# Optimization experiments

Hardware: AMD Instinct MI355X
Metric: run time of the kernel (lower is better)

## Reference

```python
import jax, jax.numpy as jnp
import numpy as np

N_NODES = 50000
N_EDGES = 800000
C_FEAT = 96
HID = 96
C_CONST = 0.005


def _psi(v):
    return jnp.sign(v) * jnp.log(jnp.abs(v) + 1.0)


def setup_inputs() -> dict:
    key = jax.random.key(0)
    ks = jax.random.split(key, 16)
    d_e_in = 2 * C_FEAT + 2
    d_h_in = 2 * C_FEAT
    def w(k, fan_in, fan_out):
        return jax.random.normal(k, (fan_in, fan_out), jnp.float32) * (1.0 / np.sqrt(fan_in))
    return {
        "x": jax.random.normal(ks[0], (N_NODES, 4), jnp.float32),
        "h": jax.random.normal(ks[1], (N_NODES, C_FEAT), jnp.float32),
        "edge_i": jax.random.randint(ks[2], (N_EDGES,), 0, N_NODES, jnp.int32),
        "edge_j": jax.random.randint(ks[3], (N_EDGES,), 0, N_NODES, jnp.int32),
        "We1": w(ks[4], d_e_in, HID), "be1": jnp.zeros((HID,), jnp.float32),
        "We2": w(ks[5], HID, HID), "be2": jnp.zeros((HID,), jnp.float32),
        "Wm": w(ks[6], HID, 1), "bm": jnp.zeros((1,), jnp.float32),
        "Wh1": w(ks[7], d_h_in, HID), "bh1": jnp.zeros((HID,), jnp.float32),
        "Wh2": w(ks[8], HID, C_FEAT), "bh2": jnp.zeros((C_FEAT,), jnp.float32),
        "Wx1": w(ks[9], HID, HID), "bx1": jnp.zeros((HID,), jnp.float32),
        "Wx2": w(ks[10], HID, 1),  # bias-free last phi_x layer
    }


def reference(x, h, edge_i, edge_j, We1, be1, We2, be2, Wm, bm,
              Wh1, bh1, Wh2, bh2, Wx1, bx1, Wx2):
    n = x.shape[0]
    x_i = x[edge_i]            # (K,4)
    x_j = x[edge_j]            # (K,4)
    # Minkowski invariants: 2*t-component - full Euclidean sum == (+,-,-,-)
    d2 = jnp.square(x_i - x_j)
    norms = 2.0 * d2[..., 0] - jnp.sum(d2, axis=-1)
    z = x_i * x_j
    prods = 2.0 * z[..., 0] - jnp.sum(z, axis=-1)
    norms = _psi(norms)[:, None]   # (K,1)
    prods = _psi(prods)[:, None]   # (K,1)

    e_in = jnp.concatenate([h[edge_i], h[edge_j], norms, prods], axis=-1)  # (K,2C+2)
    m = jax.nn.relu(jax.nn.relu(e_in @ We1 + be1) @ We2 + be2)             # (K,HID)
    w_gate = jax.nn.sigmoid(m @ Wm + bm)                                   # (K,1)

    wm = jax.ops.segment_sum(w_gate * m, edge_i, num_segments=n)          # (N,HID)
    dh = jax.nn.relu(jnp.concatenate([h, wm], axis=-1) @ Wh1 + bh1) @ Wh2 + bh2
    h_out = h + dh

    phi_x = jax.nn.relu(m @ Wx1 + bx1) @ Wx2                              # (K,1)
    vals = phi_x * x_j                                                     # (K,4)
    s = jax.ops.segment_sum(vals, edge_i, num_segments=n)                 # (N,4)
    cnt = jax.ops.segment_sum(jnp.ones((vals.shape[0],), vals.dtype), edge_i, num_segments=n)
    mean = jnp.where(cnt[:, None] > 0, s / jnp.maximum(cnt[:, None], 1.0), 0.0)
    x_out = x + C_CONST * mean
    return (h_out, x_out)
```

## Files before the change

kernel.cpp:

```cpp
#include <hip/hip_runtime.h>
#include <math.h>

#define NN 50000
#define NE 800000
#define NB 196
#define TE 128
#define AST 100

typedef __attribute__((ext_vector_type(8))) short short8v;
typedef __attribute__((ext_vector_type(4))) float f32x4;

__device__ __forceinline__ unsigned short f2bf(float f) {
  unsigned u = __float_as_uint(f);
  u += 0x7FFFu + ((u >> 16) & 1u);
  return (unsigned short)(u >> 16);
}
__device__ __forceinline__ unsigned pk2(float a, float b) {
  return (unsigned)f2bf(a) | ((unsigned)f2bf(b) << 16);
}
__device__ __forceinline__ float bflo(unsigned u) { return __uint_as_float(u << 16); }
__device__ __forceinline__ float bfhi(unsigned u) { return __uint_as_float(u & 0xFFFF0000u); }
__device__ __forceinline__ short8v pack8(float4 a, float4 b) {
  short8v r;
  r[0] = (short)f2bf(a.x); r[1] = (short)f2bf(a.y);
  r[2] = (short)f2bf(a.z); r[3] = (short)f2bf(a.w);
  r[4] = (short)f2bf(b.x); r[5] = (short)f2bf(b.y);
  r[6] = (short)f2bf(b.z); r[7] = (short)f2bf(b.w);
  return r;
}

__global__ void kprep(const int* __restrict__ ei, int* __restrict__ cnt,
                      const float* __restrict__ We1, const float* __restrict__ We2,
                      const float* __restrict__ Wx1, const float* __restrict__ Wh1,
                      const float* __restrict__ Wh2,
                      unsigned short* __restrict__ We1p, unsigned short* __restrict__ We2p,
                      unsigned short* __restrict__ Wx1p, unsigned short* __restrict__ Wh1p,
                      unsigned short* __restrict__ Wh2p) {
  const int b = blockIdx.x;
  if (b < NE / 256) {
    const int i = b * 256 + threadIdx.x;
    atomicAdd(&cnt[ei[i]], 1);
    return;
  }
  const int t = (b - NE / 256) * 256 + threadIdx.x;
  const int j = t & 7, lane = (t >> 3) & 63;
  const int kk = (lane >> 4) * 8 + j;
  const int nn = lane & 15;
  {
    const int tile = t >> 9, tk = tile / 12, tn = tile % 12;
    const int k = tk * 32 + kk, n2 = tn * 16 + nn;
    const float v = (n2 < 96) ? We1[k * 96 + n2] : We1[(96 + k) * 96 + (n2 - 96)];
    We1p[t] = f2bf(v);
  }
  {
    const int tile = t >> 9, tk = tile / 6, tn = tile % 6;
    const int k = tk * 32 + kk, n = tn * 16 + nn;
    Wh1p[t] = f2bf(Wh1[k * 96 + n]);
  }
  if (t < 9216) {
    const int tile = t >> 9, tk = tile / 6, tn = tile % 6;
    const int k = tk * 32 + kk, n = tn * 16 + nn;
    We2p[t] = f2bf(We2[k * 96 + n]);
    Wx1p[t] = f2bf(Wx1[k * 96 + n]);
    Wh2p[t] = f2bf(Wh2[k * 96 + n]);
  }
}

__global__ void kscanA(const int* __restrict__ cnt, int* __restrict__ pre,
                       int* __restrict__ bsum) {
  __shared__ int ps[256];
  const int b = blockIdx.x, t = threadIdx.x, idx = b * 256 + t;
  const int v = (idx < NN) ? cnt[idx] : 0;
  ps[t] = v;
  __syncthreads();
  for (int off = 1; off < 256; off <<= 1) {
    const int u = (t >= off) ? ps[t - off] : 0;
    __syncthreads();
    ps[t] += u;
    __syncthreads();
  }
  if (idx < NN) pre[idx] = ps[t] - v;
  if (t == 255) bsum[b] = ps[255];
}

__global__ void kscanB(const int* __restrict__ bsum, int* __restrict__ boff) {
  __shared__ int ps[256];
  const int t = threadIdx.x;
  const int v = (t < NB) ? bsum[t] : 0;
  ps[t] = v;
  __syncthreads();
  for (int off = 1; off < 256; off <<= 1) {
    const int u = (t >= off) ? ps[t - off] : 0;
    __syncthreads();
    ps[t] += u;
    __syncthreads();
  }
  if (t < NB) boff[t] = ps[t] - v;
}

__global__ void kscanC(const int* __restrict__ pre, const int* __restrict__ boff,
                       int* __restrict__ base, int* __restrict__ cursor) {
  const int b = blockIdx.x, t = threadIdx.x, idx = b * 256 + t;
  if (idx < NN) {
    const int v = pre[idx] + boff[b];
    base[idx] = v;
    cursor[idx] = v;
  }
  if (idx == 0) base[NN] = NE;
}

__global__ void kperm(const int* __restrict__ ei, const int* __restrict__ ej,
                      int* __restrict__ cursor,
                      int* __restrict__ eis, int* __restrict__ ejs) {
  const int i = blockIdx.x * 256 + threadIdx.x;
  const int vi = ei[i];
  const int pos = atomicAdd(&cursor[vi], 1);
  eis[pos] = vi;
  ejs[pos] = ej[i];
}

__global__ __launch_bounds__(256, 6) void k0_AB(const float* __restrict__ h,
                                                const unsigned short* __restrict__ We1p,
                                                unsigned short* __restrict__ Abf,
                                                unsigned short* __restrict__ Bbf) {
  __shared__ __align__(16) unsigned short outT[64 * 200];
  const int tid = threadIdx.x;
  const int nb = blockIdx.x * 64;
  const int l = tid & 63, w = tid >> 6, cg = l & 15, rg = l >> 4;
  {
    const int node = nb + w * 16 + cg;
    const int nc = node < NN ? node : NN - 1;
    short8v af[3];
    #pragma unroll
    for (int tk = 0; tk < 3; ++tk) {
      const float* p = h + (size_t)nc * 96 + tk * 32 + rg * 8;
      af[tk] = pack8(*(const float4*)p, *(const float4*)(p + 4));
    }
    const short8v* Wp = (const short8v*)We1p;
    __builtin_amdgcn_s_setprio(1);
    #pragma unroll
    for (int tn = 0; tn < 12; ++tn) {
      f32x4 acc = (f32x4){0.f, 0.f, 0.f, 0.f};
      acc = __builtin_amdgcn_mfma_f32_16x16x32_bf16(af[0], Wp[(0 * 12 + tn) * 64 + l], acc, 0, 0, 0);
      acc = __builtin_amdgcn_mfma_f32_16x16x32_bf16(af[1], Wp[(1 * 12 + tn) * 64 + l], acc, 0, 0, 0);
      acc = __builtin_amdgcn_mfma_f32_16x16x32_bf16(af[2], Wp[(2 * 12 + tn) * 64 + l], acc, 0, 0, 0);
      #pragma unroll
      for (int r = 0; r < 4; ++r)
        outT[(w * 16 + rg * 4 + r) * 200 + tn * 16 + cg] = f2bf(acc[r]);
    }
    __builtin_amdgcn_s_setprio(0);
  }
  __syncthreads();
  {
    const int e = tid & 63, q = tid >> 6;
    const int node = nb + e;
    if (node < NN) {
      const unsigned* src = (const unsigned*)outT + e * 100;
      if (q < 2) {
        uint4* dA = (uint4*)(Abf + (size_t)node * 96);
        #pragma unroll
        for (int i = 0; i < 6; ++i) dA[q * 6 + i] = *(const uint4*)(src + (q * 6 + i) * 4);
      } else {
        uint4* dB = (uint4*)(Bbf + (size_t)node * 96);
        #pragma unroll
        for (int i = 0; i < 6; ++i) dB[(q - 2) * 6 + i] = *(const uint4*)(src + 48 + ((q - 2) * 6 + i) * 4);
      }
    }
  }
}

__global__ __launch_bounds__(256, 5) void k1_edge(const float* __restrict__ x,
    const unsigned short* __restrict__ Abf, const unsigned short* __restrict__ Bbf,
    const int* __restrict__ eis, const int* __restrict__ ejs,
    const float* __restrict__ We1, const float* __restrict__ be1,
    const unsigned short* __restrict__ We2p, const float* __restrict__ be2,
    const float* __restrict__ Wm, const float* __restrict__ bm,
    const unsigned short* __restrict__ Wx1p, const float* __restrict__ bx1,
    const float* __restrict__ Wx2,
    float* __restrict__ wmo, float* __restrict__ svo) {
  __shared__ __align__(16) unsigned short actT[TE * AST];
  __shared__ float gl[TE];
  __shared__ float phil[TE];
  __shared__ __align__(16) float xjl[TE * 4];
  __shared__ int vseq[TE + 2];
  __shared__ unsigned long long bmask[2];

  const int tid = threadIdx.x;
  const float bm0 = bm[0];
  const int tb = blockIdx.x * TE;

  {
    const int e2 = tid & 127, hf = tid >> 7;
    const int fb = hf * 48;
    const int vi = eis[tb + e2], vj = ejs[tb + e2];
    const float4 xi = *(const float4*)(x + (long)vi * 4);
    const float4 xj = *(const float4*)(x + (long)vj * 4);
    if (hf == 0) {
      vseq[1 + e2] = vi;
      *(float4*)(xjl + e2 * 4) = xj;
    }
    if (tid == 0) {
      vseq[0] = (tb > 0) ? eis[tb - 1] : -1;
      vseq[TE + 1] = (tb + TE < NE) ? eis[tb + TE] : -1;
    }
    const float d0 = xi.x - xj.x, d1 = xi.y - xj.y, d2 = xi.z - xj.z, d3 = xi.w - xj.w;
    const float nrm = d0 * d0 - d1 * d1 - d2 * d2 - d3 * d3;
    const float prd = xi.x * xj.x - xi.y * xj.y - xi.z * xj.z - xi.w * xj.w;
    const float pn = copysignf(logf(fabsf(nrm) + 1.f), nrm);
    const float pp = copysignf(logf(fabsf(prd) + 1.f), prd);
    const uint4* Ar = (const uint4*)(Abf + (size_t)vi * 96 + fb);
    const uint4* Br = (const uint4*)(Bbf + (size_t)vj * 96 + fb);
    const float* wA = We1 + 192 * 96 + fb;
    const float* wB = We1 + 193 * 96 + fb;
    const float* bE = be1 + fb;
    unsigned* arow = (unsigned*)actT + e2 * (AST / 2) + hf * 24;
    #pragma unroll
    for (int c = 0; c < 6; ++c) {
      const uint4 A4 = Ar[c], B4 = Br[c];
      const unsigned au[4] = {A4.x, A4.y, A4.z, A4.w};
      const unsigned bu[4] = {B4.x, B4.y, B4.z, B4.w};
      #pragma unroll
      for (int k2 = 0; k2 < 4; ++k2) {
        const int f = c * 8 + k2 * 2;
        const float lo = fmaxf(bflo(au[k2]) + bflo(bu[k2]) + pn * wA[f] + pp * wB[f] + bE[f], 0.f);
        const float hi = fmaxf(bfhi(au[k2]) + bfhi(bu[k2]) + pn * wA[f + 1] + pp * wB[f + 1] + bE[f + 1], 0.f);
        arow[c * 4 + k2] = pk2(lo, hi);
      }
    }
  }
  __syncthreads();

  if (tid < TE) {
    const int pred = (vseq[1 + tid] != vseq[2 + tid]) ? 1 : 0;
    const unsigned long long mk = __ballot(pred);
    if ((tid & 63) == 0) bmask[tid >> 6] = mk;
  }

  const int l = tid & 63, w = tid >> 6;
  const int cg = l & 15, rg = l >> 4;
  const int r0 = w * 32;
  const short8v* Wp2 = (const short8v*)We2p;
  const short8v* Wpx = (const short8v*)Wx1p;

  {
    short8v af[2][3];
    #pragma unroll
    for (int rt = 0; rt < 2; ++rt)
      #pragma unroll
      for (int tk = 0; tk < 3; ++tk)
        af[rt][tk] = *(const short8v*)(actT + (r0 + rt * 16 + cg) * AST + tk * 32 + rg * 8);
    f32x4 acc[2][6];
    #pragma unroll
    for (int rt = 0; rt < 2; ++rt)
      #pragma unroll
      for (int tn = 0; tn < 6; ++tn) acc[rt][tn] = (f32x4){0.f, 0.f, 0.f, 0.f};
    __builtin_amdgcn_s_setprio(1);
    #pragma unroll
    for (int tk = 0; tk < 3; ++tk)
      #pragma unroll
      for (int tn = 0; tn < 6; ++tn) {
        const short8v bf = Wp2[(tk * 6 + tn) * 64 + l];
        acc[0][tn] = __builtin_amdgcn_mfma_f32_16x16x32_bf16(af[0][tk], bf, acc[0][tn], 0, 0, 0);
        acc[1][tn] = __builtin_amdgcn_mfma_f32_16x16x32_bf16(af[1][tk], bf, acc[1][tn], 0, 0, 0);
      }
    __builtin_amdgcn_s_setprio(0);
    #pragma unroll
    for (int rt = 0; rt < 2; ++rt) {
      float gp[4] = {0.f, 0.f, 0.f, 0.f};
      #pragma unroll
      for (int tn = 0; tn < 6; ++tn) {
        const int col = tn * 16 + cg;
        const float b = be2[col], wmw = Wm[col];
        #pragma unroll
        for (int r = 0; r < 4; ++r) {
          const float v = fmaxf(acc[rt][tn][r] + b, 0.f);
          gp[r] = fmaf(v, wmw, gp[r]);
          actT[(r0 + rt * 16 + rg * 4 + r) * AST + col] = (unsigned short)f2bf(v);
        }
      }
      #pragma unroll
      for (int r = 0; r < 4; ++r) {
        float s = gp[r];
        s += __shfl_xor(s, 1); s += __shfl_xor(s, 2);
        s += __shfl_xor(s, 4); s += __shfl_xor(s, 8);
        if (cg == 0) gl[r0 + rt * 16 + rg * 4 + r] = 1.f / (1.f + expf(-(s + bm0)));
      }
    }
  }


  {
    short8v af[2][3];
    #pragma unroll
    for (int rt = 0; rt < 2; ++rt)
      #pragma unroll
      for (int tk = 0; tk < 3; ++tk)
        af[rt][tk] = *(const short8v*)(actT + (r0 + rt * 16 + cg) * AST + tk * 32 + rg * 8);
    f32x4 acc[2][6];
    #pragma unroll
    for (int rt = 0; rt < 2; ++rt)
      #pragma unroll
      for (int tn = 0; tn < 6; ++tn) acc[rt][tn] = (f32x4){0.f, 0.f, 0.f, 0.f};
    __builtin_amdgcn_s_setprio(1);
    #pragma unroll
    for (int tk = 0; tk < 3; ++tk)
      #pragma unroll
      for (int tn = 0; tn < 6; ++tn) {
        const short8v bf = Wpx[(tk * 6 + tn) * 64 + l];
        acc[0][tn] = __builtin_amdgcn_mfma_f32_16x16x32_bf16(af[0][tk], bf, acc[0][tn], 0, 0, 0);
        acc[1][tn] = __builtin_amdgcn_mfma_f32_16x16x32_bf16(af[1][tk], bf, acc[1][tn], 0, 0, 0);
      }
    __builtin_amdgcn_s_setprio(0);
    #pragma unroll
    for (int rt = 0; rt < 2; ++rt) {
      float pp2[4] = {0.f, 0.f, 0.f, 0.f};
      #pragma unroll
      for (int tn = 0; tn < 6; ++tn) {
        const int col = tn * 16 + cg;
        const float b = bx1[col], wxw = Wx2[col];
        #pragma unroll
        for (int r = 0; r < 4; ++r)
          pp2[r] = fmaf(fmaxf(acc[rt][tn][r] + b, 0.f), wxw, pp2[r]);
      }
      #pragma unroll
      for (int r = 0; r < 4; ++r) {
        float s = pp2[r];
        s += __shfl_xor(s, 1); s += __shfl_xor(s, 2);
        s += __shfl_xor(s, 4); s += __shfl_xor(s, 8);
        if (cg == 0) phil[r0 + rt * 16 + rg * 4 + r] = s;
      }
    }
  }
  __syncthreads();

  if (tid < 192) {
    const int q0 = (tid >= 96) ? 1 : 0;
    const int col = tid - 96 * q0;
    #pragma unroll
    for (int pass = 0; pass < 2; ++pass) {
      const int q = q0 + 2 * pass;
      const int s_lo = q * 32, s_hi = s_lo + 32;
      const unsigned long long mk = bmask[q >> 1];
      float acc2 = 0.f;
      bool clean = (q == 0) ? (vseq[0] != vseq[1])
                            : (((bmask[(s_lo - 1) >> 6] >> ((s_lo - 1) & 63)) & 1ull) != 0);
      int e = s_lo;
      while (e < s_hi) {
        const unsigned long long rem = mk >> (e & 63);
        const int span = rem ? (int)__builtin_ctzll(rem) : 64;
        int end = e + span;
        const bool gend = (end < s_hi);
        if (end > s_hi - 1) end = s_hi - 1;
        for (int i = e; i <= end; ++i)
          acc2 = fmaf(gl[i], __uint_as_float(((unsigned)actT[i * AST + col]) << 16), acc2);
        const int node = vseq[end + 1];
        float* dst = wmo + (size_t)node * 96 + col;
        if (clean && gend) *dst = acc2; else atomicAdd(dst, acc2);
        acc2 = 0.f; clean = true;
        e = end + 1;
      }
    }
  } else if (tid < 224) {
    const int t2 = tid - 192;
    const int comp = t2 & 3, q8 = t2 >> 2;
    const int s_lo = q8 * 16, s_hi = s_lo + 16;
    const unsigned long long mk = bmask[q8 >> 2];
    float acc2 = 0.f;
    bool clean = (q8 == 0) ? (vseq[0] != vseq[1])
                           : (((bmask[(s_lo - 1) >> 6] >> ((s_lo - 1) & 63)) & 1ull) != 0);
    int e = s_lo;
    while (e < s_hi) {
      const unsigned long long rem = mk >> (e & 63);
      const int span = rem ? (int)__builtin_ctzll(rem) : 64;
      int end = e + span;
      const bool gend = (end < s_hi);
      if (end > s_hi - 1) end = s_hi - 1;
      for (int i = e; i <= end; ++i)
        acc2 = fmaf(phil[i], xjl[i * 4 + comp], acc2);
      const int node = vseq[end + 1];
      float* dst = svo + (size_t)node * 4 + comp;
      if (clean && gend) *dst = acc2; else atomicAdd(dst, acc2);
      acc2 = 0.f; clean = true;
      e = end + 1;
    }
  }
}

__global__ __launch_bounds__(256, 4) void k3ab(const float* __restrict__ h,
    const float* __restrict__ wmv,
    const unsigned short* __restrict__ Wh1p, const float* __restrict__ bh1,
    const unsigned short* __restrict__ Wh2p, const float* __restrict__ bh2,
    const float* __restrict__ x, const float* __restrict__ svm,
    const int* __restrict__ basep,
    float* __restrict__ hout, float* __restrict__ xout) {
  __shared__ __align__(16) unsigned short tmpT[64 * 104];
  __shared__ __align__(16) float oT[64 * 100];
  const int tid = threadIdx.x;
  const int nb = blockIdx.x * 64;
  const int l = tid & 63, w = tid >> 6, cg = l & 15, rg = l >> 4;
  {
    const int node = nb + w * 16 + cg;
    const int nc = node < NN ? node : NN - 1;
    short8v af[6];
    #pragma unroll
    for (int tk = 0; tk < 3; ++tk) {
      const float* p = h + (size_t)nc * 96 + tk * 32 + rg * 8;
      af[tk] = pack8(*(const float4*)p, *(const float4*)(p + 4));
      const float* pw = wmv + (size_t)nc * 96 + tk * 32 + rg * 8;
      af[3 + tk] = pack8(*(const float4*)pw, *(const float4*)(pw + 4));
    }
    const short8v* Wp = (const short8v*)Wh1p;
    __builtin_amdgcn_s_setprio(1);
    #pragma unroll
    for (int tn = 0; tn < 6; ++tn) {
      f32x4 acc = (f32x4){0.f, 0.f, 0.f, 0.f};
      #pragma unroll
      for (int tk = 0; tk < 6; ++tk)
        acc = __builtin_amdgcn_mfma_f32_16x16x32_bf16(af[tk], Wp[(tk * 6 + tn) * 64 + l], acc, 0, 0, 0);
      const int col = tn * 16 + cg;
      const float b = bh1[col];
      #pragma unroll
      for (int r = 0; r < 4; ++r)
        tmpT[(w * 16 + rg * 4 + r) * 104 + col] = f2bf(fmaxf(acc[r] + b, 0.f));
    }
    __builtin_amdgcn_s_setprio(0);
  }
  {
    const unsigned short* mr = tmpT + (w * 16 + cg) * 104;
    const short8v mf0 = *(const short8v*)(mr + rg * 8);
    const short8v mf1 = *(const short8v*)(mr + 32 + rg * 8);
    const short8v mf2 = *(const short8v*)(mr + 64 + rg * 8);
    const short8v* Wp = (const short8v*)Wh2p;
    __builtin_amdgcn_s_setprio(1);
    #pragma unroll
    for (int tn = 0; tn < 6; ++tn) {
      f32x4 acc = (f32x4){0.f, 0.f, 0.f, 0.f};
      acc = __builtin_amdgcn_mfma_f32_16x16x32_bf16(mf0, Wp[(0 * 6 + tn) * 64 + l], acc, 0, 0, 0);
      acc = __builtin_amdgcn_mfma_f32_16x16x32_bf16(mf1, Wp[(1 * 6 + tn) * 64 + l], acc, 0, 0, 0);
      acc = __builtin_amdgcn_mfma_f32_16x16x32_bf16(mf2, Wp[(2 * 6 + tn) * 64 + l], acc, 0, 0, 0);
      const int col = tn * 16 + cg;
      const float b = bh2[col];
      #pragma unroll
      for (int r = 0; r < 4; ++r)
        oT[(w * 16 + rg * 4 + r) * 100 + col] = acc[r] + b;
    }
    __builtin_amdgcn_s_setprio(0);
  }
  __syncthreads();
  {
    const int e = tid & 63, q = tid >> 6;
    const int node = nb + e;
    if (node < NN) {
      const float* src = oT + e * 100 + q * 24;
      const float* hr = h + (size_t)node * 96 + q * 24;
      float* dst = hout + (size_t)node * 96 + q * 24;
      #pragma unroll
      for (int c = 0; c < 6; ++c) {
        const float4 s = *(const float4*)(src + c * 4);
        const float4 hv = *(const float4*)(hr + c * 4);
        *(float4*)(dst + c * 4) = make_float4(hv.x + s.x, hv.y + s.y, hv.z + s.z, hv.w + s.w);
      }
    }
  }
  if (tid < 64) {
    const int node = nb + tid;
    if (node < NN) {
      const int cnt = basep[node + 1] - basep[node];
      const float inv = cnt > 0 ? 1.f / (float)cnt : 0.f;
      const float4 s4 = *(const float4*)(svm + (long)node * 4);
      const float4 xv = *(const float4*)(x + (long)node * 4);
      *(float4*)(xout + (long)node * 4) =
          make_float4(xv.x + 0.005f * s4.x * inv, xv.y + 0.005f * s4.y * inv,
                      xv.z + 0.005f * s4.z * inv, xv.w + 0.005f * s4.w * inv);
    }
  }
}

extern "C" void kernel_launch(void* const* d_in, const int* in_sizes, int n_in,
                              void* d_out, int out_size, void* d_ws, size_t ws_size,
                              hipStream_t stream) {
  const float* x   = (const float*)d_in[0];
  const float* h   = (const float*)d_in[1];
  const int*   ei  = (const int*)d_in[2];
  const int*   ej  = (const int*)d_in[3];
  const float* We1 = (const float*)d_in[4];
  const float* be1 = (const float*)d_in[5];
  const float* We2 = (const float*)d_in[6];
  const float* be2 = (const float*)d_in[7];
  const float* Wm  = (const float*)d_in[8];
  const float* bm  = (const float*)d_in[9];
  const float* Wh1 = (const float*)d_in[10];
  const float* bh1 = (const float*)d_in[11];
  const float* Wh2 = (const float*)d_in[12];
  const float* bh2 = (const float*)d_in[13];
  const float* Wx1 = (const float*)d_in[14];
  const float* bx1 = (const float*)d_in[15];
  const float* Wx2 = (const float*)d_in[16];

  char* w = (char*)d_ws;
  unsigned short* Abf  = (unsigned short*)w;
  unsigned short* Bbf  = (unsigned short*)(w + 9600000);
  float* WMv  = (float*)(w + 19200000);
  float* SvM  = (float*)(w + 38400000);
  int*   cnt  = (int*)(w + 39200000);
  int*   base = (int*)(w + 39400000);
  int*   curs = (int*)(w + 39600064);
  unsigned short* We2p = (unsigned short*)(w + 39800064);
  unsigned short* Wx1p = (unsigned short*)(w + 39818496);
  unsigned short* We1p = (unsigned short*)(w + 39836928);
  unsigned short* Wh1p = (unsigned short*)(w + 39873792);
  unsigned short* Wh2p = (unsigned short*)(w + 39910656);
  int*   eis  = (int*)(w + 39929088);
  int*   ejs  = (int*)(w + 43129088);
  int*   pre  = (int*)(w + 46329088);
  int*   bsum = (int*)(w + 46529088);
  int*   boff = (int*)(w + 46529872);

  float* hout = (float*)d_out;
  float* xout = hout + 4800000;

  hipMemsetAsync(cnt, 0, NN * sizeof(int), stream);
  hipMemsetAsync(WMv, 0, (size_t)(4800000 + 200000) * sizeof(float), stream);
  kprep<<<NE / 256 + 72, 256, 0, stream>>>(ei, cnt, We1, We2, Wx1, Wh1, Wh2,
                                           We1p, We2p, Wx1p, Wh1p, Wh2p);
  kscanA<<<NB, 256, 0, stream>>>(cnt, pre, bsum);
  kscanB<<<1, 256, 0, stream>>>(bsum, boff);
  kscanC<<<NB, 256, 0, stream>>>(pre, boff, base, curs);
  kperm<<<NE / 256, 256, 0, stream>>>(ei, ej, curs, eis, ejs);
  k0_AB<<<782, 256, 0, stream>>>(h, We1p, Abf, Bbf);
  k1_edge<<<NE / TE, 256, 0, stream>>>(x, Abf, Bbf, eis, ejs, We1, be1, We2p, be2,
                                       Wm, bm, Wx1p, bx1, Wx2, WMv, SvM);
  k3ab<<<782, 256, 0, stream>>>(h, WMv, Wh1p, bh1, Wh2p, bh2, x, SvM, base, hout, xout);
}
```

Measured before the change: 317.8 us.

## Compute first edge-MLP layer per edge via MFMA on bf16 h instead of node precompute

Removes the per-node precompute of h@We1 halves (k0_AB) and instead gathers bf16 h rows for both endpoints and runs the full first layer as a K=224 MFMA per edge, folding the psi invariants and bias into an augmented weight tile. It also packs the sorted edge indices into int2 and converts h to bf16 in the prep kernel, and drops the s_setprio hints. The goal is to cut the launch and the A/B buffer traffic. In exchange each edge does roughly twice the first-layer MFMA work, the bias and invariants are rounded to bf16, and occupancy is lowered to 4 blocks.

```diff
diff --git a/kernel.cpp b/kernel.cpp
--- a/kernel.cpp
+++ b/kernel.cpp
@@ -18,8 +18,6 @@
 __device__ __forceinline__ unsigned pk2(float a, float b) {
   return (unsigned)f2bf(a) | ((unsigned)f2bf(b) << 16);
 }
-__device__ __forceinline__ float bflo(unsigned u) { return __uint_as_float(u << 16); }
-__device__ __forceinline__ float bfhi(unsigned u) { return __uint_as_float(u & 0xFFFF0000u); }
 __device__ __forceinline__ short8v pack8(float4 a, float4 b) {
   short8v r;
   r[0] = (short)f2bf(a.x); r[1] = (short)f2bf(a.y);
@@ -30,39 +28,54 @@
 }
 
 __global__ void kprep(const int* __restrict__ ei, int* __restrict__ cnt,
-                      const float* __restrict__ We1, const float* __restrict__ We2,
-                      const float* __restrict__ Wx1, const float* __restrict__ Wh1,
-                      const float* __restrict__ Wh2,
-                      unsigned short* __restrict__ We1p, unsigned short* __restrict__ We2p,
+                      const float* __restrict__ We1, const float* __restrict__ be1,
+                      const float* __restrict__ We2, const float* __restrict__ Wx1,
+                      const float* __restrict__ Wh1, const float* __restrict__ Wh2,
+                      const float* __restrict__ h,
+                      unsigned short* __restrict__ We1xp, unsigned short* __restrict__ We2p,
                       unsigned short* __restrict__ Wx1p, unsigned short* __restrict__ Wh1p,
-                      unsigned short* __restrict__ Wh2p) {
+                      unsigned short* __restrict__ Wh2p, unsigned short* __restrict__ hbf) {
   const int b = blockIdx.x;
   if (b < NE / 256) {
     const int i = b * 256 + threadIdx.x;
     atomicAdd(&cnt[ei[i]], 1);
     return;
   }
-  const int t = (b - NE / 256) * 256 + threadIdx.x;
-  const int j = t & 7, lane = (t >> 3) & 63;
-  const int kk = (lane >> 4) * 8 + j;
-  const int nn = lane & 15;
-  {
-    const int tile = t >> 9, tk = tile / 12, tn = tile % 12;
-    const int k = tk * 32 + kk, n2 = tn * 16 + nn;
-    const float v = (n2 < 96) ? We1[k * 96 + n2] : We1[(96 + k) * 96 + (n2 - 96)];
-    We1p[t] = f2bf(v);
-  }
-  {
-    const int tile = t >> 9, tk = tile / 6, tn = tile % 6;
-    const int k = tk * 32 + kk, n = tn * 16 + nn;
-    Wh1p[t] = f2bf(Wh1[k * 96 + n]);
-  }
-  if (t < 9216) {
-    const int tile = t >> 9, tk = tile / 6, tn = tile % 6;
-    const int k = tk * 32 + kk, n = tn * 16 + nn;
-    We2p[t] = f2bf(We2[k * 96 + n]);
-    Wx1p[t] = f2bf(Wx1[k * 96 + n]);
-    Wh2p[t] = f2bf(Wh2[k * 96 + n]);
+  if (b < NE / 256 + 84) {
+    const int t = (b - NE / 256) * 256 + threadIdx.x;
+    const int j = t & 7, lane = (t >> 3) & 63;
+    const int kk = (lane >> 4) * 8 + j;
+    const int nn = lane & 15;
+    {
+      const int tile = t >> 9, tk = tile / 6, tn = tile % 6;
+      const int k = tk * 32 + kk, n = tn * 16 + nn;
+      float v = 0.f;
+      if (k < 194) v = We1[k * 96 + n];
+      else if (k == 194) v = be1[n];
+      We1xp[t] = f2bf(v);
+    }
+    if (t < 18432) {
+      const int tile = t >> 9, tk = tile / 6, tn = tile % 6;
+      const int k = tk * 32 + kk, n = tn * 16 + nn;
+      Wh1p[t] = f2bf(Wh1[k * 96 + n]);
+    }
+    if (t < 9216) {
+      const int tile = t >> 9, tk = tile / 6, tn = tile % 6;
+      const int k = tk * 32 + kk, n = tn * 16 + nn;
+      We2p[t] = f2bf(We2[k * 96 + n]);
+      Wx1p[t] = f2bf(Wx1[k * 96 + n]);
+      Wh2p[t] = f2bf(Wh2[k * 96 + n]);
+    }
+    return;
+  }
+  const int t2 = (b - NE / 256 - 84) * 256 + threadIdx.x;
+  const int base = t2 * 8;
+  if (base < NN * 96) {
+    const float4 v0 = *(const float4*)(h + base);
+    const float4 v1 = *(const float4*)(h + base + 4);
+    unsigned* dst = (unsigned*)hbf + t2 * 4;
+    dst[0] = pk2(v0.x, v0.y); dst[1] = pk2(v0.z, v0.w);
+    dst[2] = pk2(v1.x, v1.y); dst[3] = pk2(v1.z, v1.w);
   }
 }
 
@@ -110,69 +123,16 @@
 }
 
 __global__ void kperm(const int* __restrict__ ei, const int* __restrict__ ej,
-                      int* __restrict__ cursor,
-                      int* __restrict__ eis, int* __restrict__ ejs) {
+                      int* __restrict__ cursor, int2* __restrict__ ep) {
   const int i = blockIdx.x * 256 + threadIdx.x;
   const int vi = ei[i];
   const int pos = atomicAdd(&cursor[vi], 1);
-  eis[pos] = vi;
-  ejs[pos] = ej[i];
-}
-
-__global__ __launch_bounds__(256, 6) void k0_AB(const float* __restrict__ h,
-                                                const unsigned short* __restrict__ We1p,
-                                                unsigned short* __restrict__ Abf,
-                                                unsigned short* __restrict__ Bbf) {
-  __shared__ __align__(16) unsigned short outT[64 * 200];
-  const int tid = threadIdx.x;
-  const int nb = blockIdx.x * 64;
-  const int l = tid & 63, w = tid >> 6, cg = l & 15, rg = l >> 4;
-  {
-    const int node = nb + w * 16 + cg;
-    const int nc = node < NN ? node : NN - 1;
-    short8v af[3];
-    #pragma unroll
-    for (int tk = 0; tk < 3; ++tk) {
-      const float* p = h + (size_t)nc * 96 + tk * 32 + rg * 8;
-      af[tk] = pack8(*(const float4*)p, *(const float4*)(p + 4));
-    }
-    const short8v* Wp = (const short8v*)We1p;
-    __builtin_amdgcn_s_setprio(1);
-    #pragma unroll
-    for (int tn = 0; tn < 12; ++tn) {
-      f32x4 acc = (f32x4){0.f, 0.f, 0.f, 0.f};
-      acc = __builtin_amdgcn_mfma_f32_16x16x32_bf16(af[0], Wp[(0 * 12 + tn) * 64 + l], acc, 0, 0, 0);
-      acc = __builtin_amdgcn_mfma_f32_16x16x32_bf16(af[1], Wp[(1 * 12 + tn) * 64 + l], acc, 0, 0, 0);
-      acc = __builtin_amdgcn_mfma_f32_16x16x32_bf16(af[2], Wp[(2 * 12 + tn) * 64 + l], acc, 0, 0, 0);
-      #pragma unroll
-      for (int r = 0; r < 4; ++r)
-        outT[(w * 16 + rg * 4 + r) * 200 + tn * 16 + cg] = f2bf(acc[r]);
-    }
-    __builtin_amdgcn_s_setprio(0);
-  }
-  __syncthreads();
-  {
-    const int e = tid & 63, q = tid >> 6;
-    const int node = nb + e;
-    if (node < NN) {
-      const unsigned* src = (const unsigned*)outT + e * 100;
-      if (q < 2) {
-        uint4* dA = (uint4*)(Abf + (size_t)node * 96);
-        #pragma unroll
-        for (int i = 0; i < 6; ++i) dA[q * 6 + i] = *(const uint4*)(src + (q * 6 + i) * 4);
-      } else {
-        uint4* dB = (uint4*)(Bbf + (size_t)node * 96);
-        #pragma unroll
-        for (int i = 0; i < 6; ++i) dB[(q - 2) * 6 + i] = *(const uint4*)(src + 48 + ((q - 2) * 6 + i) * 4);
-      }
-    }
-  }
-}
-
-__global__ __launch_bounds__(256, 5) void k1_edge(const float* __restrict__ x,
-    const unsigned short* __restrict__ Abf, const unsigned short* __restrict__ Bbf,
-    const int* __restrict__ eis, const int* __restrict__ ejs,
-    const float* __restrict__ We1, const float* __restrict__ be1,
+  ep[pos] = make_int2(vi, ej[i]);
+}
+
+__global__ __launch_bounds__(256, 4) void k1_edge(const float* __restrict__ x,
+    const unsigned short* __restrict__ hbf, const int2* __restrict__ ep,
+    const unsigned short* __restrict__ We1xp,
     const unsigned short* __restrict__ We2p, const float* __restrict__ be2,
     const float* __restrict__ Wm, const float* __restrict__ bm,
     const unsigned short* __restrict__ Wx1p, const float* __restrict__ bx1,
@@ -183,49 +143,30 @@
   __shared__ float phil[TE];
   __shared__ __align__(16) float xjl[TE * 4];
   __shared__ int vseq[TE + 2];
+  __shared__ int vjl[TE];
+  __shared__ unsigned short pnb[TE], ppb[TE];
   __shared__ unsigned long long bmask[2];
 
   const int tid = threadIdx.x;
   const float bm0 = bm[0];
   const int tb = blockIdx.x * TE;
 
-  {
-    const int e2 = tid & 127, hf = tid >> 7;
-    const int fb = hf * 48;
-    const int vi = eis[tb + e2], vj = ejs[tb + e2];
+  if (tid < TE) {
+    const int2 v2 = ep[tb + tid];
+    const int vi = v2.x, vj = v2.y;
+    vseq[1 + tid] = vi;
+    vjl[tid] = vj;
     const float4 xi = *(const float4*)(x + (long)vi * 4);
     const float4 xj = *(const float4*)(x + (long)vj * 4);
-    if (hf == 0) {
-      vseq[1 + e2] = vi;
-      *(float4*)(xjl + e2 * 4) = xj;
-    }
-    if (tid == 0) {
-      vseq[0] = (tb > 0) ? eis[tb - 1] : -1;
-      vseq[TE + 1] = (tb + TE < NE) ? eis[tb + TE] : -1;
-    }
+    *(float4*)(xjl + tid * 4) = xj;
     const float d0 = xi.x - xj.x, d1 = xi.y - xj.y, d2 = xi.z - xj.z, d3 = xi.w - xj.w;
     const float nrm = d0 * d0 - d1 * d1 - d2 * d2 - d3 * d3;
     const float prd = xi.x * xj.x - xi.y * xj.y - xi.z * xj.z - xi.w * xj.w;
-    const float pn = copysignf(logf(fabsf(nrm) + 1.f), nrm);
-    const float pp = copysignf(logf(fabsf(prd) + 1.f), prd);
-    const uint4* Ar = (const uint4*)(Abf + (size_t)vi * 96 + fb);
-    const uint4* Br = (const uint4*)(Bbf + (size_t)vj * 96 + fb);
-    const float* wA = We1 + 192 * 96 + fb;
-    const float* wB = We1 + 193 * 96 + fb;
-    const float* bE = be1 + fb;
-    unsigned* arow = (unsigned*)actT + e2 * (AST / 2) + hf * 24;
-    #pragma unroll
-    for (int c = 0; c < 6; ++c) {
-      const uint4 A4 = Ar[c], B4 = Br[c];
-      const unsigned au[4] = {A4.x, A4.y, A4.z, A4.w};
-      const unsigned bu[4] = {B4.x, B4.y, B4.z, B4.w};
-      #pragma unroll
-      for (int k2 = 0; k2 < 4; ++k2) {
-        const int f = c * 8 + k2 * 2;
-        const float lo = fmaxf(bflo(au[k2]) + bflo(bu[k2]) + pn * wA[f] + pp * wB[f] + bE[f], 0.f);
-        const float hi = fmaxf(bfhi(au[k2]) + bfhi(bu[k2]) + pn * wA[f + 1] + pp * wB[f + 1] + bE[f + 1], 0.f);
-        arow[c * 4 + k2] = pk2(lo, hi);
-      }
+    pnb[tid] = f2bf(copysignf(logf(fabsf(nrm) + 1.f), nrm));
+    ppb[tid] = f2bf(copysignf(logf(fabsf(prd) + 1.f), prd));
+    if (tid == 0) {
+      vseq[0] = (tb > 0) ? ep[tb - 1].x : -1;
+      vseq[TE + 1] = (tb + TE < NE) ? ep[tb + TE].x : -1;
     }
   }
   __syncthreads();
@@ -239,6 +180,47 @@
   const int l = tid & 63, w = tid >> 6;
   const int cg = l & 15, rg = l >> 4;
   const int r0 = w * 32;
+
+  {
+    const short8v* W1 = (const short8v*)We1xp;
+    #pragma unroll 1
+    for (int rt = 0; rt < 2; ++rt) {
+      const int e = r0 + rt * 16 + cg;
+      const int vi = vseq[1 + e], vj = vjl[e];
+      const unsigned short* hv = hbf + (size_t)vi * 96 + rg * 8;
+      const unsigned short* hw = hbf + (size_t)vj * 96 + rg * 8;
+      short8v ha[7];
+      ha[0] = *(const short8v*)(hv);
+      ha[1] = *(const short8v*)(hv + 32);
+      ha[2] = *(const short8v*)(hv + 64);
+      ha[3] = *(const short8v*)(hw);
+      ha[4] = *(const short8v*)(hw + 32);
+      ha[5] = *(const short8v*)(hw + 64);
+      short8v tl = (short8v){0, 0, 0, 0, 0, 0, 0, 0};
+      if (rg == 0) {
+        tl[0] = (short)pnb[e];
+        tl[1] = (short)ppb[e];
+        tl[2] = (short)0x3f80;
+      }
+      ha[6] = tl;
+      f32x4 acc[6];
+      #pragma unroll
+      for (int tn = 0; tn < 6; ++tn) acc[tn] = (f32x4){0.f, 0.f, 0.f, 0.f};
+      #pragma unroll
+      for (int tk = 0; tk < 7; ++tk)
+        #pragma unroll
+        for (int tn = 0; tn < 6; ++tn)
+          acc[tn] = __builtin_amdgcn_mfma_f32_16x16x32_bf16(ha[tk], W1[(tk * 6 + tn) * 64 + l], acc[tn], 0, 0, 0);
+      #pragma unroll
+      for (int tn = 0; tn < 6; ++tn) {
+        const int col = tn * 16 + cg;
+        #pragma unroll
+        for (int r = 0; r < 4; ++r)
+          actT[(r0 + rt * 16 + rg * 4 + r) * AST + col] = f2bf(fmaxf(acc[tn][r], 0.f));
+      }
+    }
+  }
+
   const short8v* Wp2 = (const short8v*)We2p;
   const short8v* Wpx = (const short8v*)Wx1p;
 
@@ -254,7 +236,6 @@
     for (int rt = 0; rt < 2; ++rt)
       #pragma unroll
       for (int tn = 0; tn < 6; ++tn) acc[rt][tn] = (f32x4){0.f, 0.f, 0.f, 0.f};
-    __builtin_amdgcn_s_setprio(1);
     #pragma unroll
     for (int tk = 0; tk < 3; ++tk)
       #pragma unroll
@@ -263,7 +244,6 @@
         acc[0][tn] = __builtin_amdgcn_mfma_f32_16x16x32_bf16(af[0][tk], bf, acc[0][tn], 0, 0, 0);
         acc[1][tn] = __builtin_amdgcn_mfma_f32_16x16x32_bf16(af[1][tk], bf, acc[1][tn], 0, 0, 0);
       }
-    __builtin_amdgcn_s_setprio(0);
     #pragma unroll
     for (int rt = 0; rt < 2; ++rt) {
       float gp[4] = {0.f, 0.f, 0.f, 0.f};
@@ -288,7 +268,6 @@
     }
   }
 
-
   {
     short8v af[2][3];
     #pragma unroll
@@ -301,7 +280,6 @@
     for (int rt = 0; rt < 2; ++rt)
       #pragma unroll
       for (int tn = 0; tn < 6; ++tn) acc[rt][tn] = (f32x4){0.f, 0.f, 0.f, 0.f};
-    __builtin_amdgcn_s_setprio(1);
     #pragma unroll
     for (int tk = 0; tk < 3; ++tk)
       #pragma unroll
@@ -310,7 +288,6 @@
         acc[0][tn] = __builtin_amdgcn_mfma_f32_16x16x32_bf16(af[0][tk], bf, acc[0][tn], 0, 0, 0);
         acc[1][tn] = __builtin_amdgcn_mfma_f32_16x16x32_bf16(af[1][tk], bf, acc[1][tn], 0, 0, 0);
       }
-    __builtin_amdgcn_s_setprio(0);
     #pragma unroll
     for (int rt = 0; rt < 2; ++rt) {
       float pp2[4] = {0.f, 0.f, 0.f, 0.f};
@@ -410,7 +387,6 @@
       af[3 + tk] = pack8(*(const float4*)pw, *(const float4*)(pw + 4));
     }
     const short8v* Wp = (const short8v*)Wh1p;
-    __builtin_amdgcn_s_setprio(1);
     #pragma unroll
     for (int tn = 0; tn < 6; ++tn) {
       f32x4 acc = (f32x4){0.f, 0.f, 0.f, 0.f};
@@ -423,7 +399,6 @@
       for (int r = 0; r < 4; ++r)
         tmpT[(w * 16 + rg * 4 + r) * 104 + col] = f2bf(fmaxf(acc[r] + b, 0.f));
     }
-    __builtin_amdgcn_s_setprio(0);
   }
   {
     const unsigned short* mr = tmpT + (w * 16 + cg) * 104;
@@ -431,7 +406,6 @@
     const short8v mf1 = *(const short8v*)(mr + 32 + rg * 8);
     const short8v mf2 = *(const short8v*)(mr + 64 + rg * 8);
     const short8v* Wp = (const short8v*)Wh2p;
-    __builtin_amdgcn_s_setprio(1);
     #pragma unroll
     for (int tn = 0; tn < 6; ++tn) {
       f32x4 acc = (f32x4){0.f, 0.f, 0.f, 0.f};
@@ -444,7 +418,6 @@
       for (int r = 0; r < 4; ++r)
         oT[(w * 16 + rg * 4 + r) * 100 + col] = acc[r] + b;
     }
-    __builtin_amdgcn_s_setprio(0);
   }
   __syncthreads();
   {
@@ -498,37 +471,34 @@
   const float* Wx2 = (const float*)d_in[16];
 
   char* w = (char*)d_ws;
-  unsigned short* Abf  = (unsigned short*)w;
-  unsigned short* Bbf  = (unsigned short*)(w + 9600000);
-  float* WMv  = (float*)(w + 19200000);
-  float* SvM  = (float*)(w + 38400000);
-  int*   cnt  = (int*)(w + 39200000);
-  int*   base = (int*)(w + 39400000);
-  int*   curs = (int*)(w + 39600064);
-  unsigned short* We2p = (unsigned short*)(w + 39800064);
-  unsigned short* Wx1p = (unsigned short*)(w + 39818496);
-  unsigned short* We1p = (unsigned short*)(w + 39836928);
-  unsigned short* Wh1p = (unsigned short*)(w + 39873792);
-  unsigned short* Wh2p = (unsigned short*)(w + 39910656);
-  int*   eis  = (int*)(w + 39929088);
-  int*   ejs  = (int*)(w + 43129088);
-  int*   pre  = (int*)(w + 46329088);
-  int*   bsum = (int*)(w + 46529088);
-  int*   boff = (int*)(w + 46529872);
+  unsigned short* hbf  = (unsigned short*)w;
+  float* WMv  = (float*)(w + 9600000);
+  float* SvM  = (float*)(w + 28800000);
+  int*   cnt  = (int*)(w + 29600000);
+  int*   base = (int*)(w + 29800000);
+  int*   curs = (int*)(w + 30000064);
+  unsigned short* We1xp = (unsigned short*)(w + 30200064);
+  unsigned short* We2p  = (unsigned short*)(w + 30243072);
+  unsigned short* Wx1p  = (unsigned short*)(w + 30261504);
+  unsigned short* Wh1p  = (unsigned short*)(w + 30279936);
+  unsigned short* Wh2p  = (unsigned short*)(w + 30316800);
+  int2*  epb  = (int2*)(w + 30335232);
+  int*   pre  = (int*)(w + 36735232);
+  int*   bsum = (int*)(w + 36935232);
+  int*   boff = (int*)(w + 36936064);
 
   float* hout = (float*)d_out;
   float* xout = hout + 4800000;
 
   hipMemsetAsync(cnt, 0, NN * sizeof(int), stream);
   hipMemsetAsync(WMv, 0, (size_t)(4800000 + 200000) * sizeof(float), stream);
-  kprep<<<NE / 256 + 72, 256, 0, stream>>>(ei, cnt, We1, We2, Wx1, Wh1, Wh2,
-                                           We1p, We2p, Wx1p, Wh1p, Wh2p);
+  kprep<<<NE / 256 + 84 + 2344, 256, 0, stream>>>(ei, cnt, We1, be1, We2, Wx1, Wh1, Wh2, h,
+                                                  We1xp, We2p, Wx1p, Wh1p, Wh2p, hbf);
   kscanA<<<NB, 256, 0, stream>>>(cnt, pre, bsum);
   kscanB<<<1, 256, 0, stream>>>(bsum, boff);
   kscanC<<<NB, 256, 0, stream>>>(pre, boff, base, curs);
-  kperm<<<NE / 256, 256, 0, stream>>>(ei, ej, curs, eis, ejs);
-  k0_AB<<<782, 256, 0, stream>>>(h, We1p, Abf, Bbf);
-  k1_edge<<<NE / TE, 256, 0, stream>>>(x, Abf, Bbf, eis, ejs, We1, be1, We2p, be2,
+  kperm<<<NE / 256, 256, 0, stream>>>(ei, ej, curs, epb);
+  k1_edge<<<NE / TE, 256, 0, stream>>>(x, hbf, epb, We1xp, We2p, be2,
                                        Wm, bm, Wx1p, bx1, Wx2, WMv, SvM);
   k3ab<<<782, 256, 0, stream>>>(h, WMv, Wh1p, bh1, Wh2p, bh2, x, SvM, base, hout, xout);
 }
```

Result: slower. 602.1 us (+89.5%).
